# Optimization experiments

Hardware: AMD Instinct MI355X
Metric: run time of the kernel (lower is better)

The kernel has to match this reference:

```python
import jax, jax.numpy as jnp
import numpy as np

H = 1024      # hidden_size
V = 50257     # output_size (vocab)


def setup_inputs() -> dict:
    key = jax.random.key(0)
    ks = jax.random.split(key, 9)
    s = 1.0 / np.sqrt(H)
    return {
        "input_ids": jax.random.randint(ks[0], (1,), 0, V, dtype=jnp.int64)
        if jax.config.jax_enable_x64 else jax.random.randint(ks[0], (1,), 0, V, dtype=jnp.int32),
        "hidden": jax.random.normal(ks[1], (1, 1, H), dtype=jnp.float32),
        "emb": jax.random.normal(ks[2], (V, H), dtype=jnp.float32),
        "W_ih": jax.random.uniform(ks[3], (3 * H, H), jnp.float32, -s, s),
        "W_hh": jax.random.uniform(ks[4], (3 * H, H), jnp.float32, -s, s),
        "b_ih": jax.random.uniform(ks[5], (3 * H,), jnp.float32, -s, s),
        "b_hh": jax.random.uniform(ks[6], (3 * H,), jnp.float32, -s, s),
        "W_out": jax.random.uniform(ks[7], (V, H), jnp.float32, -s, s),
        "b_out": jax.random.uniform(ks[8], (V,), jnp.float32, -s, s),
    }


def gru_cell(x, h, W_ih, W_hh, b_ih, b_hh):
    # x, h: [B, H]; PyTorch GRU gate ordering: r, z, n
    gi = x @ W_ih.T + b_ih           # [B, 3H]
    gh = h @ W_hh.T + b_hh           # [B, 3H]
    i_r, i_z, i_n = jnp.split(gi, 3, axis=-1)
    h_r, h_z, h_n = jnp.split(gh, 3, axis=-1)
    r = jax.nn.sigmoid(i_r + h_r)
    z = jax.nn.sigmoid(i_z + h_z)
    n = jnp.tanh(i_n + r * h_n)
    return (1.0 - z) * n + z * h


def reference(input_ids, hidden, emb, W_ih, W_hh, b_ih, b_hh, W_out, b_out):
    # embedding lookup -> [1, 1, H] (seq=1, batch=1)
    x = emb[input_ids].reshape(1, 1, H)
    x = jax.nn.relu(x)
    # single-step, single-layer GRU (n_layers = 1 in the original intent)
    h_new = gru_cell(x[0], hidden[0], W_ih, W_hh, b_ih, b_hh)   # [1, H]
    hidden_out = h_new[None]                                    # [1, 1, H]
    logits = h_new @ W_out.T + b_out                            # [1, V]
    logp = jax.nn.log_softmax(logits, axis=-1)
    return logp, hidden_out
```

## Files before the change

kernel.cpp:

```cpp
#include <hip/hip_runtime.h>
#include <math.h>

#define H 1024
#define V 50257
#define G 3072
#define NB_LOGITS 3142

__device__ __forceinline__ float wave_reduce_sum(float v) {
#pragma unroll
    for (int off = 32; off >= 1; off >>= 1)
        v += __shfl_xor(v, off, 64);
    return v;
}

__device__ __forceinline__ void sm_merge(float& m, float& s, float mi, float si) {
    if (mi > m) {
        s = s * expf(m - mi) + si;
        m = mi;
    } else if (si > 0.f) {
        s += si * expf(mi - m);
    }
}

__global__ __launch_bounds__(256) void gates_kernel(
    const int* __restrict__ ids, const float* __restrict__ emb,
    const float* __restrict__ hidden,
    const float* __restrict__ W_ih, const float* __restrict__ W_hh,
    const float* __restrict__ b_ih, const float* __restrict__ b_hh,
    float* __restrict__ gi, float* __restrict__ gh)
{
    const int wave = threadIdx.x >> 6;
    const int lane = threadIdx.x & 63;
    const int row  = blockIdx.x * 4 + wave;
    if (row >= G) return;

    const int id = ids[0];
    const float4* xr = (const float4*)(emb + (size_t)id * H);
    const float4* hr = (const float4*)hidden;
    const float4* wi = (const float4*)(W_ih + (size_t)row * H);
    const float4* wh = (const float4*)(W_hh + (size_t)row * H);

    float ai = 0.f, ah = 0.f;
#pragma unroll
    for (int it = 0; it < 4; ++it) {
        const int k = it * 64 + lane;
        float4 x4 = xr[k];
        x4.x = fmaxf(x4.x, 0.f); x4.y = fmaxf(x4.y, 0.f);
        x4.z = fmaxf(x4.z, 0.f); x4.w = fmaxf(x4.w, 0.f);
        const float4 h4  = hr[k];
        const float4 wi4 = wi[k];
        const float4 wh4 = wh[k];
        ai += wi4.x * x4.x + wi4.y * x4.y + wi4.z * x4.z + wi4.w * x4.w;
        ah += wh4.x * h4.x + wh4.y * h4.y + wh4.z * h4.z + wh4.w * h4.w;
    }
    ai = wave_reduce_sum(ai);
    ah = wave_reduce_sum(ah);
    if (lane == 0) {
        gi[row] = ai + b_ih[row];
        gh[row] = ah + b_hh[row];
    }
}

__global__ __launch_bounds__(1024) void gru_combine_kernel(
    const float* __restrict__ gi, const float* __restrict__ gh,
    const float* __restrict__ hidden,
    float* __restrict__ hnew, float* __restrict__ out_hidden)
{
    const int j = threadIdx.x;
    const float ir = gi[j],       hr = gh[j];
    const float iz = gi[H + j],   hz = gh[H + j];
    const float in_ = gi[2*H + j], hn = gh[2*H + j];
    const float r = 1.f / (1.f + expf(-(ir + hr)));
    const float z = 1.f / (1.f + expf(-(iz + hz)));
    const float n = tanhf(in_ + r * hn);
    const float h = hidden[j];
    const float out = (1.f - z) * n + z * h;
    hnew[j] = out;
    out_hidden[j] = out;
}

__global__ __launch_bounds__(256) void logits_kernel(
    const float* __restrict__ hnew, const float* __restrict__ W_out,
    const float* __restrict__ b_out, float* __restrict__ logits,
    float* __restrict__ pmax, float* __restrict__ psum)
{
    __shared__ float hs[H];
    __shared__ float wm[4], wsv[4];

    for (int i = threadIdx.x; i < H; i += 256) hs[i] = hnew[i];
    __syncthreads();

    const int wave = threadIdx.x >> 6;
    const int lane = threadIdx.x & 63;
    const int base = blockIdx.x * 16 + wave * 4;
    const float4* h4 = (const float4*)hs;

    float m = -INFINITY, s = 0.f;
#pragma unroll
    for (int r = 0; r < 4; ++r) {
        const int row = base + r;
        if (row >= V) break;
        const float4* w = (const float4*)(W_out + (size_t)row * H);
        float acc = 0.f;
#pragma unroll
        for (int it = 0; it < 4; ++it) {
            const int k = it * 64 + lane;
            const float4 w4 = w[k];
            const float4 x4 = h4[k];
            acc += w4.x * x4.x + w4.y * x4.y + w4.z * x4.z + w4.w * x4.w;
        }
        acc = wave_reduce_sum(acc);
        if (lane == 0) {
            const float logit = acc + b_out[row];
            logits[row] = logit;
            sm_merge(m, s, logit, 1.f);
        }
    }
    if (lane == 0) { wm[wave] = m; wsv[wave] = s; }
    __syncthreads();
    if (threadIdx.x == 0) {
        float M = wm[0], S = wsv[0];
#pragma unroll
        for (int w2 = 1; w2 < 4; ++w2) sm_merge(M, S, wm[w2], wsv[w2]);
        pmax[blockIdx.x] = M;
        psum[blockIdx.x] = S;
    }
}

__global__ __launch_bounds__(256) void reduce_kernel(
    const float* __restrict__ pmax, const float* __restrict__ psum,
    float* __restrict__ total)
{
    __shared__ float wm[4], wsv[4];
    const int tid = threadIdx.x;
    float m = -INFINITY, s = 0.f;
    for (int i = tid; i < NB_LOGITS; i += 256)
        sm_merge(m, s, pmax[i], psum[i]);
#pragma unroll
    for (int off = 32; off >= 1; off >>= 1) {
        const float mo = __shfl_xor(m, off, 64);
        const float so = __shfl_xor(s, off, 64);
        sm_merge(m, s, mo, so);
    }
    if ((tid & 63) == 0) { wm[tid >> 6] = m; wsv[tid >> 6] = s; }
    __syncthreads();
    if (tid == 0) {
        float M = wm[0], S = wsv[0];
#pragma unroll
        for (int w2 = 1; w2 < 4; ++w2) sm_merge(M, S, wm[w2], wsv[w2]);
        *total = M + logf(S);
    }
}

__global__ __launch_bounds__(256) void logp_kernel(
    float* __restrict__ out, const float* __restrict__ total)
{
    const float t = *total;
    const int v = blockIdx.x * 256 + threadIdx.x;
    if (v < V) out[v] -= t;
}

extern "C" void kernel_launch(void* const* d_in, const int* in_sizes, int n_in,
                              void* d_out, int out_size, void* d_ws, size_t ws_size,
                              hipStream_t stream) {
    const int*   ids    = (const int*)  d_in[0];
    const float* hidden = (const float*)d_in[1];
    const float* emb    = (const float*)d_in[2];
    const float* W_ih   = (const float*)d_in[3];
    const float* W_hh   = (const float*)d_in[4];
    const float* b_ih   = (const float*)d_in[5];
    const float* b_hh   = (const float*)d_in[6];
    const float* W_out  = (const float*)d_in[7];
    const float* b_out  = (const float*)d_in[8];

    float* out = (float*)d_out;

    float* ws    = (float*)d_ws;
    float* gi    = ws;
    float* gh    = ws + G;
    float* hnew  = ws + 2 * G;
    float* pmax  = ws + 2 * G + H;
    float* psum  = pmax + NB_LOGITS;
    float* total = psum + NB_LOGITS;

    gates_kernel<<<G / 4, 256, 0, stream>>>(ids, emb, hidden, W_ih, W_hh,
                                            b_ih, b_hh, gi, gh);
    gru_combine_kernel<<<1, 1024, 0, stream>>>(gi, gh, hidden, hnew, out + V);
    logits_kernel<<<NB_LOGITS, 256, 0, stream>>>(hnew, W_out, b_out, out, pmax, psum);
    reduce_kernel<<<1, 256, 0, stream>>>(pmax, psum, total);
    logp_kernel<<<(V + 255) / 256, 256, 0, stream>>>(out, total);
}
```

Baseline: 55.01 us.

## Fuse GRU gates with combine and reduction with log-softmax subtraction

The gate matvec and the GRU combine now run in one kernel, with one block per hidden unit computing all six dot products and applying the nonlinearities, so the gi/gh round trip and a separate single-block launch are gone. The softmax partial reduction and the logp subtraction are merged into one 64-block kernel in which every block redundantly reduces the partials and then subtracts over a strided range. This drops the chain from five launches to three, at the cost of repeating the reduction work in every block.

```diff
diff --git a/kernel.cpp b/kernel.cpp
--- a/kernel.cpp
+++ b/kernel.cpp
@@ -3,8 +3,8 @@
 
 #define H 1024
 #define V 50257
-#define G 3072
 #define NB_LOGITS 3142
+#define NB_FINAL 64
 
 __device__ __forceinline__ float wave_reduce_sum(float v) {
 #pragma unroll
@@ -22,61 +22,61 @@
     }
 }
 
-__global__ __launch_bounds__(256) void gates_kernel(
+__global__ __launch_bounds__(256) void gru_fused_kernel(
     const int* __restrict__ ids, const float* __restrict__ emb,
     const float* __restrict__ hidden,
     const float* __restrict__ W_ih, const float* __restrict__ W_hh,
     const float* __restrict__ b_ih, const float* __restrict__ b_hh,
-    float* __restrict__ gi, float* __restrict__ gh)
+    float* __restrict__ hnew, float* __restrict__ out_hidden)
 {
-    const int wave = threadIdx.x >> 6;
-    const int lane = threadIdx.x & 63;
-    const int row  = blockIdx.x * 4 + wave;
-    if (row >= G) return;
+    const int j = blockIdx.x;
+    const int t = threadIdx.x;
+    const int wave = t >> 6;
+    const int lane = t & 63;
 
     const int id = ids[0];
     const float4* xr = (const float4*)(emb + (size_t)id * H);
     const float4* hr = (const float4*)hidden;
-    const float4* wi = (const float4*)(W_ih + (size_t)row * H);
-    const float4* wh = (const float4*)(W_hh + (size_t)row * H);
 
-    float ai = 0.f, ah = 0.f;
+    float4 x4 = xr[t];
+    x4.x = fmaxf(x4.x, 0.f); x4.y = fmaxf(x4.y, 0.f);
+    x4.z = fmaxf(x4.z, 0.f); x4.w = fmaxf(x4.w, 0.f);
+    const float4 h4 = hr[t];
+
+    float acc[6];
 #pragma unroll
-    for (int it = 0; it < 4; ++it) {
-        const int k = it * 64 + lane;
-        float4 x4 = xr[k];
-        x4.x = fmaxf(x4.x, 0.f); x4.y = fmaxf(x4.y, 0.f);
-        x4.z = fmaxf(x4.z, 0.f); x4.w = fmaxf(x4.w, 0.f);
-        const float4 h4  = hr[k];
-        const float4 wi4 = wi[k];
-        const float4 wh4 = wh[k];
-        ai += wi4.x * x4.x + wi4.y * x4.y + wi4.z * x4.z + wi4.w * x4.w;
-        ah += wh4.x * h4.x + wh4.y * h4.y + wh4.z * h4.z + wh4.w * h4.w;
+    for (int g = 0; g < 3; ++g) {
+        const size_t row = (size_t)g * H + j;
+        const float4 wi4 = ((const float4*)(W_ih + row * H))[t];
+        const float4 wh4 = ((const float4*)(W_hh + row * H))[t];
+        acc[2*g]   = wi4.x * x4.x + wi4.y * x4.y + wi4.z * x4.z + wi4.w * x4.w;
+        acc[2*g+1] = wh4.x * h4.x + wh4.y * h4.y + wh4.z * h4.z + wh4.w * h4.w;
     }
-    ai = wave_reduce_sum(ai);
-    ah = wave_reduce_sum(ah);
+#pragma unroll
+    for (int g = 0; g < 6; ++g) acc[g] = wave_reduce_sum(acc[g]);
+
+    __shared__ float red[4][6];
     if (lane == 0) {
-        gi[row] = ai + b_ih[row];
-        gh[row] = ah + b_hh[row];
+#pragma unroll
+        for (int g = 0; g < 6; ++g) red[wave][g] = acc[g];
     }
-}
-
-__global__ __launch_bounds__(1024) void gru_combine_kernel(
-    const float* __restrict__ gi, const float* __restrict__ gh,
-    const float* __restrict__ hidden,
-    float* __restrict__ hnew, float* __restrict__ out_hidden)
-{
-    const int j = threadIdx.x;
-    const float ir = gi[j],       hr = gh[j];
-    const float iz = gi[H + j],   hz = gh[H + j];
-    const float in_ = gi[2*H + j], hn = gh[2*H + j];
-    const float r = 1.f / (1.f + expf(-(ir + hr)));
-    const float z = 1.f / (1.f + expf(-(iz + hz)));
-    const float n = tanhf(in_ + r * hn);
-    const float h = hidden[j];
-    const float out = (1.f - z) * n + z * h;
-    hnew[j] = out;
-    out_hidden[j] = out;
+    __syncthreads();
+    if (t == 0) {
+        float tt[6];
+#pragma unroll
+        for (int g = 0; g < 6; ++g)
+            tt[g] = red[0][g] + red[1][g] + red[2][g] + red[3][g];
+        const float ir = tt[0] + b_ih[j],       hr_ = tt[1] + b_hh[j];
+        const float iz = tt[2] + b_ih[H + j],   hz  = tt[3] + b_hh[H + j];
+        const float in_ = tt[4] + b_ih[2*H + j], hn = tt[5] + b_hh[2*H + j];
+        const float r = 1.f / (1.f + expf(-(ir + hr_)));
+        const float z = 1.f / (1.f + expf(-(iz + hz)));
+        const float n = tanhf(in_ + r * hn);
+        const float h = hidden[j];
+        const float out = (1.f - z) * n + z * h;
+        hnew[j] = out;
+        out_hidden[j] = out;
+    }
 }
 
 __global__ __launch_bounds__(256) void logits_kernel(
@@ -127,12 +127,14 @@
     }
 }
 
-__global__ __launch_bounds__(256) void reduce_kernel(
+__global__ __launch_bounds__(256) void finalize_kernel(
     const float* __restrict__ pmax, const float* __restrict__ psum,
-    float* __restrict__ total)
+    float* __restrict__ out)
 {
     __shared__ float wm[4], wsv[4];
+    __shared__ float total_s;
     const int tid = threadIdx.x;
+
     float m = -INFINITY, s = 0.f;
     for (int i = tid; i < NB_LOGITS; i += 256)
         sm_merge(m, s, pmax[i], psum[i]);
@@ -148,16 +150,13 @@
         float M = wm[0], S = wsv[0];
 #pragma unroll
         for (int w2 = 1; w2 < 4; ++w2) sm_merge(M, S, wm[w2], wsv[w2]);
-        *total = M + logf(S);
+        total_s = M + logf(S);
     }
-}
+    __syncthreads();
+    const float t = total_s;
 
-__global__ __launch_bounds__(256) void logp_kernel(
-    float* __restrict__ out, const float* __restrict__ total)
-{
-    const float t = *total;
-    const int v = blockIdx.x * 256 + threadIdx.x;
-    if (v < V) out[v] -= t;
+    for (int v = blockIdx.x * 256 + tid; v < V; v += NB_FINAL * 256)
+        out[v] -= t;
 }
 
 extern "C" void kernel_launch(void* const* d_in, const int* in_sizes, int n_in,
@@ -176,17 +175,12 @@
     float* out = (float*)d_out;
 
     float* ws    = (float*)d_ws;
-    float* gi    = ws;
-    float* gh    = ws + G;
-    float* hnew  = ws + 2 * G;
-    float* pmax  = ws + 2 * G + H;
+    float* hnew  = ws;
+    float* pmax  = ws + H;
     float* psum  = pmax + NB_LOGITS;
-    float* total = psum + NB_LOGITS;
 
-    gates_kernel<<<G / 4, 256, 0, stream>>>(ids, emb, hidden, W_ih, W_hh,
-                                            b_ih, b_hh, gi, gh);
-    gru_combine_kernel<<<1, 1024, 0, stream>>>(gi, gh, hidden, hnew, out + V);
+    gru_fused_kernel<<<H, 256, 0, stream>>>(ids, emb, hidden, W_ih, W_hh,
+                                            b_ih, b_hh, hnew, out + V);
     logits_kernel<<<NB_LOGITS, 256, 0, stream>>>(hnew, W_out, b_out, out, pmax, psum);
-    reduce_kernel<<<1, 256, 0, stream>>>(pmax, psum, total);
-    logp_kernel<<<(V + 255) / 256, 256, 0, stream>>>(out, total);
+    finalize_kernel<<<NB_FINAL, 256, 0, stream>>>(pmax, psum, out);
 }
```

Result: faster. 52.85 us (-3.9%).
